# Kernel tuning notes

Measured on AMD Instinct MI355X. Metric: run time of the kernel, lower is better.

## Reference

```python
import math
import jax, jax.numpy as jnp
import numpy as np

IN_DIM = 1024
OUT_DIM = 1024
K = 32
N_BANDS = 3
TOTAL_K = K * N_BANDS
LAYER_IDX = 0
NUM_LAYERS = 1
SCALE = math.sqrt(2.0 / (IN_DIM + OUT_DIM))


def _make_pos():
    l_val = (LAYER_IDX + 1) / (NUM_LAYERS + 1)
    i_idx = (jnp.arange(IN_DIM, dtype=jnp.float32) + 1) / (IN_DIM + 1)
    j_idx = (jnp.arange(OUT_DIM, dtype=jnp.float32) + 1) / (OUT_DIM + 1)
    ii, jj = jnp.meshgrid(i_idx, j_idx, indexing='ij')
    pos = jnp.stack([ii, jj, jnp.full_like(ii, l_val)], axis=-1)
    return pos.reshape(-1, 3)  # (in_dim*out_dim, 3)


def setup_inputs() -> dict:
    key = jax.random.key(0)
    kx, ko, kp, ka = jax.random.split(key, 4)
    x = jax.random.normal(kx, (4096, IN_DIM), dtype=jnp.float32)
    # omega with per-band scaling (1 + band*3), matching the torch init
    band_scales = jnp.repeat(1.0 + 3.0 * jnp.arange(N_BANDS, dtype=jnp.float32), K)
    omega = jax.random.normal(ko, (TOTAL_K, 3), dtype=jnp.float32) * band_scales[:, None]
    phi = jax.random.normal(kp, (TOTAL_K,), dtype=jnp.float32) * math.pi
    alpha = jax.random.normal(ka, (2 * TOTAL_K,), dtype=jnp.float32) * 0.01 / (1.0 + jnp.arange(2 * TOTAL_K, dtype=jnp.float32))
    bias = jnp.zeros((OUT_DIM,), dtype=jnp.float32)
    pos = _make_pos()
    return {"x": x, "omega": omega, "phi": phi, "alpha": alpha, "bias": bias, "pos": pos}


def reference(x, omega, phi, alpha, bias, pos):
    # args: (in*out, total_k)
    args = pos @ omega.T + phi
    # features @ alpha == sin(args)@alpha[:K2//2] + cos(args)@alpha[K2//2:]
    a_sin, a_cos = alpha[:TOTAL_K], alpha[TOTAL_K:]
    w_flat = jnp.sin(args) @ a_sin + jnp.cos(args) @ a_cos  # (in*out,)
    # torch: w = flat.reshape(in, out).T * scale; F.linear(x, w) = x @ w.T
    w_t = w_flat.reshape(IN_DIM, OUT_DIM) * SCALE  # == w.T
    return x @ w_t + bias
```

## Files before the change

### kernel.cpp

```cpp
#include <hip/hip_runtime.h>
#include <hip/hip_bf16.h>
#include <math.h>


#define IN_DIM   1024
#define OUT_DIM  1024
#define NBANDS   96
#define KTAB     192
#define MX       4096
#define SCALE_W  0.03125f
#define NSPLIT   4

typedef __bf16 bf16x8 __attribute__((ext_vector_type(8)));
typedef float  f32x4  __attribute__((ext_vector_type(4)));

#define AS1 __attribute__((address_space(1)))
#define AS3 __attribute__((address_space(3)))

__device__ __forceinline__ void gload_lds16(const void* g, void* l) {
  __builtin_amdgcn_global_load_lds((AS1 void*)(g), (AS3 void*)(l), 16, 0, 0);
}

__device__ __forceinline__ unsigned short bf16bits(float f) {
  __hip_bfloat16 b = __float2bfloat16(f);
  return *(unsigned short*)&b;
}

__global__ void build_tables(const float* __restrict__ omega,
                             const float* __restrict__ phi,
                             const float* __restrict__ alpha,
                             __hip_bfloat16* __restrict__ TaT,
                             __hip_bfloat16* __restrict__ Tb) {
  const int t = blockIdx.x;
  const float ox = omega[3 * t], oy = omega[3 * t + 1], oz = omega[3 * t + 2];
  const float uc = oz * 0.5f + phi[t];
  const float as_ = alpha[t], ac = alpha[NBANDS + t];
#pragma unroll
  for (int s = 0; s < 4; ++s) {
    const int i = s * 256 + threadIdx.x;
    const float coord = (float)(i + 1) / 1025.0f;
    float su, cu;
    sincosf(ox * coord + uc, &su, &cu);
    const float P = SCALE_W * (as_ * su + ac * cu);
    const float Q = SCALE_W * (as_ * cu - ac * su);
    TaT[(size_t)(2 * t) * IN_DIM + i]     = __float2bfloat16(P);
    TaT[(size_t)(2 * t + 1) * IN_DIM + i] = __float2bfloat16(Q);
    float sv, cv;
    sincosf(oy * coord, &sv, &cv);
    Tb[(size_t)i * KTAB + 2 * t]     = __float2bfloat16(cv);
    Tb[(size_t)i * KTAB + 2 * t + 1] = __float2bfloat16(sv);
  }
}

__global__ __launch_bounds__(512)
void gemm_xta(const float* __restrict__ X,
              const __hip_bfloat16* __restrict__ TaT,
              float* __restrict__ Pp) {
  __shared__ __align__(16) __hip_bfloat16 As[64 * 32];
  __shared__ __align__(16) __hip_bfloat16 Bs[192 * 32];
  const int tid  = threadIdx.x;
  const int lane = tid & 63;
  const int wave = tid >> 6;
  const int wr = wave >> 2;
  const int wc = wave & 3;
  const int m0  = blockIdx.y * 64;
  const int ks0 = blockIdx.z * (IN_DIM / NSPLIT);

  f32x4 acc[2][3] = {};
  const int lr = lane & 15;
  const int lk = (lane >> 4) * 8;

  for (int k0 = 0; k0 < IN_DIM / NSPLIT; k0 += 32) {
    {
      const int r = tid >> 3;
      const int c4 = tid & 7;
      float4 v = *(const float4*)(X + (size_t)(m0 + r) * IN_DIM + ks0 + k0 + c4 * 4);
      ushort4 o;
      o.x = bf16bits(v.x); o.y = bf16bits(v.y);
      o.z = bf16bits(v.z); o.w = bf16bits(v.w);
      *(ushort4*)((char*)As + (size_t)r * 64 + c4 * 8) = o;
    }
    {
      const int r = tid >> 2, c16 = tid & 3;
      gload_lds16(TaT + (size_t)r * IN_DIM + ks0 + k0 + c16 * 8,
                  (char*)Bs + (size_t)tid * 16);
      if (tid < 256) {
        const int c2 = 512 + tid;
        const int r2 = c2 >> 2, c162 = c2 & 3;
        gload_lds16(TaT + (size_t)r2 * IN_DIM + ks0 + k0 + c162 * 8,
                    (char*)Bs + (size_t)c2 * 16);
      }
    }
    __syncthreads();

    bf16x8 af[2], bfr[3];
#pragma unroll
    for (int mi = 0; mi < 2; ++mi)
      af[mi] = *(const bf16x8*)&As[(wr * 32 + mi * 16 + lr) * 32 + lk];
#pragma unroll
    for (int ni = 0; ni < 3; ++ni)
      bfr[ni] = *(const bf16x8*)&Bs[(wc * 48 + ni * 16 + lr) * 32 + lk];
#pragma unroll
    for (int mi = 0; mi < 2; ++mi)
#pragma unroll
      for (int ni = 0; ni < 3; ++ni)
        acc[mi][ni] = __builtin_amdgcn_mfma_f32_16x16x32_bf16(
            af[mi], bfr[ni], acc[mi][ni], 0, 0, 0);
    __syncthreads();
  }

  float* P = Pp + (size_t)blockIdx.z * (MX * KTAB);
#pragma unroll
  for (int mi = 0; mi < 2; ++mi)
#pragma unroll
    for (int ni = 0; ni < 3; ++ni)
#pragma unroll
      for (int r = 0; r < 4; ++r) {
        const int row = m0 + wr * 32 + mi * 16 + (lane >> 4) * 4 + r;
        const int col = wc * 48 + ni * 16 + lr;
        P[(size_t)row * KTAB + col] = acc[mi][ni][r];
      }
}

__global__ void reduce_y(const float* __restrict__ Pp,
                         __hip_bfloat16* __restrict__ Y) {
  const int i = (blockIdx.x * 256 + threadIdx.x) * 4;
  const int S = MX * KTAB;
  float4 a = *(const float4*)(Pp + i);
  float4 b = *(const float4*)(Pp + S + i);
  float4 c = *(const float4*)(Pp + 2 * S + i);
  float4 d = *(const float4*)(Pp + 3 * S + i);
  ushort4 o;
  o.x = bf16bits(a.x + b.x + c.x + d.x);
  o.y = bf16bits(a.y + b.y + c.y + d.y);
  o.z = bf16bits(a.z + b.z + c.z + d.z);
  o.w = bf16bits(a.w + b.w + c.w + d.w);
  *(ushort4*)(Y + i) = o;
}

__global__ __launch_bounds__(256)
void gemm_out(const __hip_bfloat16* __restrict__ Y,
              const __hip_bfloat16* __restrict__ Tb,
              float* __restrict__ out,
              const float* __restrict__ bias) {
  __shared__ __align__(16) __hip_bfloat16 As[64 * 32];
  __shared__ __align__(16) __hip_bfloat16 Bs[128 * 32];
  const int tid  = threadIdx.x;
  const int lane = tid & 63;
  const int wave = tid >> 6;
  const int wr = wave >> 1;
  const int wc = wave & 1;
  const int m0 = blockIdx.y * 64;
  const int n0 = blockIdx.x * 128;

  f32x4 acc[2][4] = {};
  const int lr = lane & 15;
  const int lk = (lane >> 4) * 8;

  for (int k0 = 0; k0 < KTAB; k0 += 32) {
    {
      const int r = tid >> 2, c16 = tid & 3;
      gload_lds16(Y + (size_t)(m0 + r) * KTAB + k0 + c16 * 8,
                  (char*)As + (size_t)tid * 16);
    }
#pragma unroll
    for (int q = 0; q < 2; ++q) {
      const int f = q * 256 + tid;
      const int r = f >> 2, c16 = f & 3;
      gload_lds16(Tb + (size_t)(n0 + r) * KTAB + k0 + c16 * 8,
                  (char*)Bs + (size_t)f * 16);
    }
    __syncthreads();

    bf16x8 af[2], bfr[4];
#pragma unroll
    for (int mi = 0; mi < 2; ++mi)
      af[mi] = *(const bf16x8*)&As[(wr * 32 + mi * 16 + lr) * 32 + lk];
#pragma unroll
    for (int ni = 0; ni < 4; ++ni)
      bfr[ni] = *(const bf16x8*)&Bs[(wc * 64 + ni * 16 + lr) * 32 + lk];
#pragma unroll
    for (int mi = 0; mi < 2; ++mi)
#pragma unroll
      for (int ni = 0; ni < 4; ++ni)
        acc[mi][ni] = __builtin_amdgcn_mfma_f32_16x16x32_bf16(
            af[mi], bfr[ni], acc[mi][ni], 0, 0, 0);
    __syncthreads();
  }

#pragma unroll
  for (int mi = 0; mi < 2; ++mi)
#pragma unroll
    for (int ni = 0; ni < 4; ++ni)
#pragma unroll
      for (int r = 0; r < 4; ++r) {
        const int row = m0 + wr * 32 + mi * 16 + (lane >> 4) * 4 + r;
        const int col = n0 + wc * 64 + ni * 16 + lr;
        out[(size_t)row * OUT_DIM + col] = acc[mi][ni][r] + bias[col];
      }
}

extern "C" void kernel_launch(void* const* d_in, const int* in_sizes, int n_in,
                              void* d_out, int out_size, void* d_ws, size_t ws_size,
                              hipStream_t stream) {
  const float* x     = (const float*)d_in[0];
  const float* omega = (const float*)d_in[1];
  const float* phi   = (const float*)d_in[2];
  const float* alpha = (const float*)d_in[3];
  const float* bias  = (const float*)d_in[4];
  float* out = (float*)d_out;
  (void)in_sizes; (void)n_in; (void)out_size; (void)ws_size;

  char* ws = (char*)d_ws;
  float* Pp           = (float*)(ws);
  __hip_bfloat16* Y   = (__hip_bfloat16*)(ws + 12582912);
  __hip_bfloat16* TaT = (__hip_bfloat16*)(ws + 14155776);
  __hip_bfloat16* Tb  = (__hip_bfloat16*)(ws + 14548992);

  build_tables<<<dim3(NBANDS), dim3(256), 0, stream>>>(omega, phi, alpha, TaT, Tb);
  gemm_xta<<<dim3(1, MX / 64, NSPLIT), dim3(512), 0, stream>>>(x, TaT, Pp);
  reduce_y<<<dim3((MX * KTAB) / (256 * 4)), dim3(256), 0, stream>>>(Pp, Y);
  gemm_out<<<dim3(OUT_DIM / 128, MX / 64), dim3(256), 0, stream>>>(Y, Tb, out, bias);
}
```

Baseline: 102.4 us.

## Double-buffer LDS with 64-wide K tiles in both GEMMs and parallelize table build

Both GEMM kernels now use double-buffered shared-memory tiles with K=64 per stage. The next tile is prefetched while MFMAs run on the current one, and the number of barriers drops by half. gemm_xta shrinks to 32-row tiles with 256 threads, which doubles the grid, and build_tables spreads its loop across a second grid dimension. The aim is to hide global-load latency and raise parallelism, at the cost of more LDS per block and possibly lower occupancy.

```diff
diff --git a/kernel.cpp b/kernel.cpp
--- a/kernel.cpp
+++ b/kernel.cpp
@@ -32,80 +32,97 @@
                              __hip_bfloat16* __restrict__ TaT,
                              __hip_bfloat16* __restrict__ Tb) {
   const int t = blockIdx.x;
+  const int i = blockIdx.y * 256 + threadIdx.x;
   const float ox = omega[3 * t], oy = omega[3 * t + 1], oz = omega[3 * t + 2];
   const float uc = oz * 0.5f + phi[t];
   const float as_ = alpha[t], ac = alpha[NBANDS + t];
-#pragma unroll
-  for (int s = 0; s < 4; ++s) {
-    const int i = s * 256 + threadIdx.x;
-    const float coord = (float)(i + 1) / 1025.0f;
-    float su, cu;
-    sincosf(ox * coord + uc, &su, &cu);
-    const float P = SCALE_W * (as_ * su + ac * cu);
-    const float Q = SCALE_W * (as_ * cu - ac * su);
-    TaT[(size_t)(2 * t) * IN_DIM + i]     = __float2bfloat16(P);
-    TaT[(size_t)(2 * t + 1) * IN_DIM + i] = __float2bfloat16(Q);
-    float sv, cv;
-    sincosf(oy * coord, &sv, &cv);
-    Tb[(size_t)i * KTAB + 2 * t]     = __float2bfloat16(cv);
-    Tb[(size_t)i * KTAB + 2 * t + 1] = __float2bfloat16(sv);
-  }
-}
-
-__global__ __launch_bounds__(512)
+  const float coord = (float)(i + 1) / 1025.0f;
+  float su, cu;
+  sincosf(ox * coord + uc, &su, &cu);
+  TaT[(size_t)(2 * t) * IN_DIM + i]     = __float2bfloat16(SCALE_W * (as_ * su + ac * cu));
+  TaT[(size_t)(2 * t + 1) * IN_DIM + i] = __float2bfloat16(SCALE_W * (as_ * cu - ac * su));
+  float sv, cv;
+  sincosf(oy * coord, &sv, &cv);
+  Tb[(size_t)i * KTAB + 2 * t]     = __float2bfloat16(cv);
+  Tb[(size_t)i * KTAB + 2 * t + 1] = __float2bfloat16(sv);
+}
+
+__global__ __launch_bounds__(256)
 void gemm_xta(const float* __restrict__ X,
               const __hip_bfloat16* __restrict__ TaT,
               float* __restrict__ Pp) {
-  __shared__ __align__(16) __hip_bfloat16 As[64 * 32];
-  __shared__ __align__(16) __hip_bfloat16 Bs[192 * 32];
+  __shared__ __align__(16) __hip_bfloat16 As[2][32 * 64];
+  __shared__ __align__(16) __hip_bfloat16 Bs[2][192 * 64];
   const int tid  = threadIdx.x;
   const int lane = tid & 63;
-  const int wave = tid >> 6;
-  const int wr = wave >> 2;
-  const int wc = wave & 3;
-  const int m0  = blockIdx.y * 64;
-  const int ks0 = blockIdx.z * (IN_DIM / NSPLIT);
-
-  f32x4 acc[2][3] = {};
+  const int wc   = tid >> 6;
+  const int m0   = blockIdx.y * 32;
+  const int ks0  = blockIdx.z * (IN_DIM / NSPLIT);
   const int lr = lane & 15;
   const int lk = (lane >> 4) * 8;
 
-  for (int k0 = 0; k0 < IN_DIM / NSPLIT; k0 += 32) {
-    {
-      const int r = tid >> 3;
-      const int c4 = tid & 7;
-      float4 v = *(const float4*)(X + (size_t)(m0 + r) * IN_DIM + ks0 + k0 + c4 * 4);
+  const float* xbase = X + (size_t)m0 * IN_DIM + ks0;
+  const __hip_bfloat16* bbase = TaT + ks0;
+
+  f32x4 acc[2][3] = {};
+
+  auto ALOAD = [&](int t, float4* a) {
+#pragma unroll
+    for (int q = 0; q < 2; ++q) {
+      const int f = q * 256 + tid;
+      const int r = f >> 4, c4 = f & 15;
+      a[q] = *(const float4*)(xbase + (size_t)r * IN_DIM + t * 64 + c4 * 4);
+    }
+  };
+  auto AWRITE = [&](int buf, const float4* a) {
+#pragma unroll
+    for (int q = 0; q < 2; ++q) {
+      const int f = q * 256 + tid;
+      const int r = f >> 4, c4 = f & 15;
       ushort4 o;
-      o.x = bf16bits(v.x); o.y = bf16bits(v.y);
-      o.z = bf16bits(v.z); o.w = bf16bits(v.w);
-      *(ushort4*)((char*)As + (size_t)r * 64 + c4 * 8) = o;
-    }
-    {
-      const int r = tid >> 2, c16 = tid & 3;
-      gload_lds16(TaT + (size_t)r * IN_DIM + ks0 + k0 + c16 * 8,
-                  (char*)Bs + (size_t)tid * 16);
-      if (tid < 256) {
-        const int c2 = 512 + tid;
-        const int r2 = c2 >> 2, c162 = c2 & 3;
-        gload_lds16(TaT + (size_t)r2 * IN_DIM + ks0 + k0 + c162 * 8,
-                    (char*)Bs + (size_t)c2 * 16);
-      }
-    }
-    __syncthreads();
-
-    bf16x8 af[2], bfr[3];
-#pragma unroll
-    for (int mi = 0; mi < 2; ++mi)
-      af[mi] = *(const bf16x8*)&As[(wr * 32 + mi * 16 + lr) * 32 + lk];
-#pragma unroll
-    for (int ni = 0; ni < 3; ++ni)
-      bfr[ni] = *(const bf16x8*)&Bs[(wc * 48 + ni * 16 + lr) * 32 + lk];
-#pragma unroll
-    for (int mi = 0; mi < 2; ++mi)
+      o.x = bf16bits(a[q].x); o.y = bf16bits(a[q].y);
+      o.z = bf16bits(a[q].z); o.w = bf16bits(a[q].w);
+      *(ushort4*)((char*)&As[buf][0] + r * 128 + c4 * 8) = o;
+    }
+  };
+  auto BSTAGE = [&](int t, int buf) {
+#pragma unroll
+    for (int q = 0; q < 6; ++q) {
+      const int f = q * 256 + tid;
+      const int r = f >> 3, g = f & 7;
+      gload_lds16(bbase + (size_t)r * IN_DIM + t * 64 + g * 8,
+                  (char*)&Bs[buf][0] + (size_t)f * 16);
+    }
+  };
+  auto COMPUTE = [&](int buf) {
+#pragma unroll
+    for (int kk = 0; kk < 2; ++kk) {
+      bf16x8 af[2], bfr[3];
+#pragma unroll
+      for (int mi = 0; mi < 2; ++mi)
+        af[mi] = *(const bf16x8*)&As[buf][(mi * 16 + lr) * 64 + kk * 32 + lk];
 #pragma unroll
       for (int ni = 0; ni < 3; ++ni)
-        acc[mi][ni] = __builtin_amdgcn_mfma_f32_16x16x32_bf16(
-            af[mi], bfr[ni], acc[mi][ni], 0, 0, 0);
+        bfr[ni] = *(const bf16x8*)&Bs[buf][(wc * 48 + ni * 16 + lr) * 64 + kk * 32 + lk];
+#pragma unroll
+      for (int mi = 0; mi < 2; ++mi)
+#pragma unroll
+        for (int ni = 0; ni < 3; ++ni)
+          acc[mi][ni] = __builtin_amdgcn_mfma_f32_16x16x32_bf16(
+              af[mi], bfr[ni], acc[mi][ni], 0, 0, 0);
+    }
+  };
+
+  float4 a0[2];
+  ALOAD(0, a0); BSTAGE(0, 0); AWRITE(0, a0);
+  __syncthreads();
+#pragma unroll
+  for (int t = 0; t < 4; ++t) {
+    const int cur = t & 1;
+    float4 an[2];
+    if (t < 3) { ALOAD(t + 1, an); BSTAGE(t + 1, cur ^ 1); }
+    COMPUTE(cur);
+    if (t < 3) AWRITE(cur ^ 1, an);
     __syncthreads();
   }
 
@@ -116,7 +133,7 @@
     for (int ni = 0; ni < 3; ++ni)
 #pragma unroll
       for (int r = 0; r < 4; ++r) {
-        const int row = m0 + wr * 32 + mi * 16 + (lane >> 4) * 4 + r;
+        const int row = m0 + mi * 16 + (lane >> 4) * 4 + r;
         const int col = wc * 48 + ni * 16 + lr;
         P[(size_t)row * KTAB + col] = acc[mi][ni][r];
       }
@@ -143,8 +160,8 @@
               const __hip_bfloat16* __restrict__ Tb,
               float* __restrict__ out,
               const float* __restrict__ bias) {
-  __shared__ __align__(16) __hip_bfloat16 As[64 * 32];
-  __shared__ __align__(16) __hip_bfloat16 Bs[128 * 32];
+  __shared__ __align__(16) __hip_bfloat16 As[2][64 * 64];
+  __shared__ __align__(16) __hip_bfloat16 Bs[2][128 * 64];
   const int tid  = threadIdx.x;
   const int lane = tid & 63;
   const int wave = tid >> 6;
@@ -152,39 +169,55 @@
   const int wc = wave & 1;
   const int m0 = blockIdx.y * 64;
   const int n0 = blockIdx.x * 128;
-
-  f32x4 acc[2][4] = {};
   const int lr = lane & 15;
   const int lk = (lane >> 4) * 8;
 
-  for (int k0 = 0; k0 < KTAB; k0 += 32) {
-    {
-      const int r = tid >> 2, c16 = tid & 3;
-      gload_lds16(Y + (size_t)(m0 + r) * KTAB + k0 + c16 * 8,
-                  (char*)As + (size_t)tid * 16);
-    }
+  f32x4 acc[2][4] = {};
+
+  auto ASTAGE = [&](int t, int buf) {
 #pragma unroll
     for (int q = 0; q < 2; ++q) {
       const int f = q * 256 + tid;
-      const int r = f >> 2, c16 = f & 3;
-      gload_lds16(Tb + (size_t)(n0 + r) * KTAB + k0 + c16 * 8,
-                  (char*)Bs + (size_t)f * 16);
-    }
-    __syncthreads();
-
-    bf16x8 af[2], bfr[4];
-#pragma unroll
-    for (int mi = 0; mi < 2; ++mi)
-      af[mi] = *(const bf16x8*)&As[(wr * 32 + mi * 16 + lr) * 32 + lk];
-#pragma unroll
-    for (int ni = 0; ni < 4; ++ni)
-      bfr[ni] = *(const bf16x8*)&Bs[(wc * 64 + ni * 16 + lr) * 32 + lk];
-#pragma unroll
-    for (int mi = 0; mi < 2; ++mi)
+      const int r = f >> 3, g = f & 7;
+      gload_lds16(Y + (size_t)(m0 + r) * KTAB + t * 64 + g * 8,
+                  (char*)&As[buf][0] + (size_t)f * 16);
+    }
+  };
+  auto BSTAGE = [&](int t, int buf) {
+#pragma unroll
+    for (int q = 0; q < 4; ++q) {
+      const int f = q * 256 + tid;
+      const int r = f >> 3, g = f & 7;
+      gload_lds16(Tb + (size_t)(n0 + r) * KTAB + t * 64 + g * 8,
+                  (char*)&Bs[buf][0] + (size_t)f * 16);
+    }
+  };
+  auto COMPUTE = [&](int buf) {
+#pragma unroll
+    for (int kk = 0; kk < 2; ++kk) {
+      bf16x8 af[2], bfr[4];
+#pragma unroll
+      for (int mi = 0; mi < 2; ++mi)
+        af[mi] = *(const bf16x8*)&As[buf][(wr * 32 + mi * 16 + lr) * 64 + kk * 32 + lk];
 #pragma unroll
       for (int ni = 0; ni < 4; ++ni)
-        acc[mi][ni] = __builtin_amdgcn_mfma_f32_16x16x32_bf16(
-            af[mi], bfr[ni], acc[mi][ni], 0, 0, 0);
+        bfr[ni] = *(const bf16x8*)&Bs[buf][(wc * 64 + ni * 16 + lr) * 64 + kk * 32 + lk];
+#pragma unroll
+      for (int mi = 0; mi < 2; ++mi)
+#pragma unroll
+        for (int ni = 0; ni < 4; ++ni)
+          acc[mi][ni] = __builtin_amdgcn_mfma_f32_16x16x32_bf16(
+              af[mi], bfr[ni], acc[mi][ni], 0, 0, 0);
+    }
+  };
+
+  ASTAGE(0, 0); BSTAGE(0, 0);
+  __syncthreads();
+#pragma unroll
+  for (int t = 0; t < 3; ++t) {
+    const int cur = t & 1;
+    if (t < 2) { ASTAGE(t + 1, cur ^ 1); BSTAGE(t + 1, cur ^ 1); }
+    COMPUTE(cur);
     __syncthreads();
   }
 
@@ -217,8 +250,8 @@
   __hip_bfloat16* TaT = (__hip_bfloat16*)(ws + 14155776);
   __hip_bfloat16* Tb  = (__hip_bfloat16*)(ws + 14548992);
 
-  build_tables<<<dim3(NBANDS), dim3(256), 0, stream>>>(omega, phi, alpha, TaT, Tb);
-  gemm_xta<<<dim3(1, MX / 64, NSPLIT), dim3(512), 0, stream>>>(x, TaT, Pp);
+  build_tables<<<dim3(NBANDS, 4), dim3(256), 0, stream>>>(omega, phi, alpha, TaT, Tb);
+  gemm_xta<<<dim3(1, MX / 32, NSPLIT), dim3(256), 0, stream>>>(x, TaT, Pp);
   reduce_y<<<dim3((MX * KTAB) / (256 * 4)), dim3(256), 0, stream>>>(Pp, Y);
   gemm_out<<<dim3(OUT_DIM / 128, MX / 64), dim3(256), 0, stream>>>(Y, Tb, out, bias);
 }
```

After: 99.03 us. 3.3% less time.
